# Kernel optimization log

Measured on AMD Instinct MI355X. Metric: run time of the kernel, lower is better.

## Reference

```python
import jax, jax.numpy as jnp
import numpy as np

N_TV_ITER = 20      # fixed Chambolle iteration count (skimage early-stops via eps; fixed for jit)
TV_WEIGHT = 0.1


def _div(p):
    # negative adjoint of forward-difference gradient (skimage convention)
    d = -(p[0] + p[1])
    d = d.at[1:, :].add(p[0, :-1, :])
    d = d.at[:, 1:].add(p[1, :, :-1])
    return d


def tv_chambolle_2d(image):
    """skimage.restoration.denoise_tv_chambolle on a single 2D image, weight=0.1."""
    tau = 0.25  # 1 / (2 * ndim)

    def step(p, _):
        out = image + _div(p)
        gy = jnp.zeros_like(out).at[:-1, :].set(out[1:, :] - out[:-1, :])
        gx = jnp.zeros_like(out).at[:, :-1].set(out[:, 1:] - out[:, :-1])
        norm = jnp.sqrt(gy * gy + gx * gx)
        g = jnp.stack([gy, gx])
        p = (p - tau * g) / (1.0 + (tau / TV_WEIGHT) * norm)
        return p, None

    p0 = jnp.zeros((2,) + image.shape, image.dtype)
    p, _ = jax.lax.scan(step, p0, None, length=N_TV_ITER)
    return image + _div(p)


def tv_denoise(img):  # [B,C,H,W], vmapped over B*C (replaces the CPU python loop)
    B, C, H, W = img.shape
    out = jax.vmap(tv_chambolle_2d)(img.reshape(B * C, H, W))
    return out.reshape(B, C, H, W)


def conv(x, w, stride=1, groups=1):
    pad = w.shape[2] // 2  # 'same'-style padding for odd kernels, 0 for 1x1
    return jax.lax.conv_general_dilated(
        x, w, (stride, stride), [(pad, pad), (pad, pad)],
        dimension_numbers=('NCHW', 'OIHW', 'NCHW'),
        feature_group_count=groups)


def haar_ll(x):
    # one level of pywt wavedec2('haar') LL band: 0.5 * sum over each 2x2 block
    return 0.5 * (x[..., ::2, ::2] + x[..., ::2, 1::2] + x[..., 1::2, ::2] + x[..., 1::2, 1::2])


def backbone(x, stem_w, dw_pw):
    # stride-32, 1280-channel EfficientNet-B0-style feature extractor
    x = jax.nn.silu(conv(x, stem_w, stride=2))
    for dw, pw in dw_pw:
        x = jax.nn.silu(conv(x, dw, stride=2, groups=dw.shape[0]))
        x = jax.nn.silu(conv(x, pw))
    return x


def setup_inputs() -> dict:
    key = jax.random.key(0)
    ks = jax.random.split(key, 16)
    B, H, W = 4, 512, 512

    def w(k, o, i, kh, kw):
        return jax.random.normal(k, (o, i, kh, kw), jnp.float32) * (1.0 / np.sqrt(i * kh * kw))

    return {
        "img": jax.random.normal(ks[0], (B, 1, H, W), jnp.float32),
        "stem_w": w(ks[1], 32, 1, 3, 3),
        "dw1_w": w(ks[2], 32, 1, 3, 3),  "pw1_w": w(ks[3], 64, 32, 1, 1),
        "dw2_w": w(ks[4], 64, 1, 3, 3),  "pw2_w": w(ks[5], 128, 64, 1, 1),
        "dw3_w": w(ks[6], 128, 1, 3, 3), "pw3_w": w(ks[7], 256, 128, 1, 1),
        "dw4_w": w(ks[8], 256, 1, 3, 3), "pw4_w": w(ks[9], 512, 256, 1, 1),
        "head_w": w(ks[10], 1280, 512, 1, 1),
        "proj_w": w(ks[11], 64, 1280, 1, 1),
        "proj_b": jnp.zeros((64,), jnp.float32),
        "final_w": w(ks[12], 1, 64, 1, 1),
        "final_b": jnp.zeros((1,), jnp.float32),
    }


def reference(img, stem_w, dw1_w, pw1_w, dw2_w, pw2_w, dw3_w, pw3_w, dw4_w, pw4_w,
              head_w, proj_w, proj_b, final_w, final_b):
    B, C, H, W = img.shape
    x = tv_denoise(img)                                     # fused TV Chambolle
    x = backbone(x, stem_w, [(dw1_w, pw1_w), (dw2_w, pw2_w), (dw3_w, pw3_w), (dw4_w, pw4_w)])
    x = jax.nn.silu(conv(x, head_w))                        # [B,1280,H/32,W/32]
    x = conv(x, proj_w) + proj_b[None, :, None, None]       # [B,64,H/32,W/32]
    x = jax.image.resize(x, (B, 64, H, W), method='bilinear')  # align_corners=False semantics
    ll = haar_ll(haar_ll(x))                                # 2-level Haar LL: [B,64,H/4,W/4]
    out = conv(ll, final_w) + final_b[None, :, None, None]  # [B,1,H/4,W/4]
    return out
```

## Files before the change

### kernel.cpp

```cpp
#include <hip/hip_runtime.h>
#include <math.h>

constexpr int BATCH = 4;
constexpr int IMG_H = 512, IMG_W = 512;
constexpr int IMG_HW = IMG_H * IMG_W;
constexpr int PSTR = BATCH * IMG_HW;

constexpr size_t O_PA   = 0;
constexpr size_t O_PB   = O_PA + 2 * (size_t)PSTR;
constexpr size_t O_DEN  = O_PB + 2 * (size_t)PSTR;
constexpr size_t O_A1   = O_DEN + (size_t)PSTR;
constexpr size_t O_A2   = O_A1 + 8388608;
constexpr size_t O_WT1  = O_A2 + 2097152;
constexpr size_t O_WT2  = O_WT1 + 32 * 64;
constexpr size_t O_WT3  = O_WT2 + 64 * 128;
constexpr size_t O_WT4  = O_WT3 + 128 * 256;
constexpr size_t O_WTH  = O_WT4 + 256 * 512;
constexpr size_t O_WCOMB= O_WTH + 512 * 1280;
constexpr size_t O_BCOMB= O_WCOMB + 1280;
constexpr size_t O_S    = O_BCOMB + 4;
constexpr size_t WS_FLOATS = O_S + 1024;

__device__ __forceinline__ float fast_rcp(float x) { return __builtin_amdgcn_rcpf(x); }
__device__ __forceinline__ float fast_sqrt(float x) { return __builtin_amdgcn_sqrtf(x); }
__device__ __forceinline__ float silu_f(float x) {
    float e = __builtin_amdgcn_exp2f(-1.44269504088896f * x);
    return x * fast_rcp(1.0f + e);
}
__device__ __forceinline__ int clampi(int v, int lo, int hi) {
    return v < lo ? lo : (v > hi ? hi : v);
}

template <int NST, bool FIRST, bool LAST>
__global__ __launch_bounds__(512) void tv_reg(const float* __restrict__ img,
                                              const float* __restrict__ pin,
                                              float* __restrict__ pout) {
    constexpr int ROWS = 7, NW = 8, HL = 10, TC = 44, TR = 32;
    __shared__ float bndP[512], bndO[512];
    const int tid = threadIdx.x;
    const int lane = tid & 63, w = tid >> 6;
    const int b = blockIdx.z;
    const int r0 = blockIdx.y * TR, c0 = blockIdx.x * TC;
    const int gj = c0 - HL + lane;
    const int gjc = clampi(gj, 0, 511);
    const int gib = r0 - HL + w * ROWS;
    const float* I = img + b * IMG_HW;
    const bool interior = (r0 - HL >= 1) && (r0 + NW * ROWS - HL <= 511) &&
                          (c0 - HL >= 1) && (c0 + 64 - HL <= 511);

    float rim[ROWS], rp0[ROWS], rp1[ROWS], ro[ROWS];
#pragma unroll
    for (int k = 0; k < ROWS; ++k) {
        int gi = clampi(gib + k, 0, 511);
        rim[k] = I[(gi << 9) + gjc];
    }
    if (!FIRST) {
        const float* P0 = pin + b * IMG_HW;
        const float* P1 = pin + PSTR + b * IMG_HW;
#pragma unroll
        for (int k = 0; k < ROWS; ++k) {
            int gi = clampi(gib + k, 0, 511);
            rp0[k] = P0[(gi << 9) + gjc];
            rp1[k] = P1[(gi << 9) + gjc];
        }
    }
    const bool gjpos = (gj > 0), gjlt = (gj < 511);

    int s0 = 0;
    if (FIRST) {
        bndO[tid] = rim[0];
        __syncthreads();
        float odn = (w < NW - 1) ? bndO[tid + 64] : 0.0f;
        if (interior) {
#pragma unroll
            for (int k = 0; k < ROWS; ++k) {
                float oR = __shfl_down(rim[k], 1);
                float od = (k < ROWS - 1) ? rim[k + 1] : odn;
                float gy = od - rim[k];
                float gx = oR - rim[k];
                float inv = fast_rcp(fmaf(2.5f, fast_sqrt(fmaf(gy, gy, gx * gx)), 1.0f));
                rp0[k] = -0.25f * gy * inv;
                rp1[k] = -0.25f * gx * inv;
            }
        } else {
#pragma unroll
            for (int k = 0; k < ROWS; ++k) {
                float oR = __shfl_down(rim[k], 1);
                float od = (k < ROWS - 1) ? rim[k + 1] : odn;
                int gi = gib + k;
                float gy = (gi < 511) ? od - rim[k] : 0.0f;
                float gx = gjlt ? oR - rim[k] : 0.0f;
                float inv = fast_rcp(fmaf(2.5f, fast_sqrt(fmaf(gy, gy, gx * gx)), 1.0f));
                rp0[k] = -0.25f * gy * inv;
                rp1[k] = -0.25f * gx * inv;
            }
        }
        s0 = 1;
    }

    for (int s = s0; s < NST; ++s) {
        bndP[tid] = rp0[ROWS - 1];
        __syncthreads();
        float pup0 = (w > 0) ? bndP[tid - 64] : 0.0f;
        if (interior) {
#pragma unroll
            for (int k = 0; k < ROWS; ++k) {
                float p1l = __shfl_up(rp1[k], 1);
                float pup = (k > 0) ? rp0[k - 1] : pup0;
                ro[k] = rim[k] - rp0[k] - rp1[k] + pup + p1l;
            }
            bndO[tid] = ro[0];
            __syncthreads();
            float odn = (w < NW - 1) ? bndO[tid + 64] : 0.0f;
#pragma unroll
            for (int k = 0; k < ROWS; ++k) {
                float oR = __shfl_down(ro[k], 1);
                float od = (k < ROWS - 1) ? ro[k + 1] : odn;
                float gy = od - ro[k];
                float gx = oR - ro[k];
                float inv = fast_rcp(fmaf(2.5f, fast_sqrt(fmaf(gy, gy, gx * gx)), 1.0f));
                rp0[k] = (rp0[k] - 0.25f * gy) * inv;
                rp1[k] = (rp1[k] - 0.25f * gx) * inv;
            }
        } else {
#pragma unroll
            for (int k = 0; k < ROWS; ++k) {
                float p1l = __shfl_up(rp1[k], 1);
                float o = rim[k] - rp0[k] - rp1[k];
                float pup = (k > 0) ? rp0[k - 1] : pup0;
                int gi = gib + k;
                if (gi > 0) o += pup;
                if (gjpos) o += p1l;
                ro[k] = o;
            }
            bndO[tid] = ro[0];
            __syncthreads();
            float odn = (w < NW - 1) ? bndO[tid + 64] : 0.0f;
#pragma unroll
            for (int k = 0; k < ROWS; ++k) {
                float oR = __shfl_down(ro[k], 1);
                float od = (k < ROWS - 1) ? ro[k + 1] : odn;
                int gi = gib + k;
                float gy = (gi < 511) ? od - ro[k] : 0.0f;
                float gx = gjlt ? oR - ro[k] : 0.0f;
                float inv = fast_rcp(fmaf(2.5f, fast_sqrt(fmaf(gy, gy, gx * gx)), 1.0f));
                rp0[k] = (rp0[k] - 0.25f * gy) * inv;
                rp1[k] = (rp1[k] - 0.25f * gx) * inv;
            }
        }
    }

    const bool cst = (lane >= HL && lane < HL + TC && gj < 512);
    if (LAST) {
        bndP[tid] = rp0[ROWS - 1];
        __syncthreads();
        float pup0 = (w > 0) ? bndP[tid - 64] : 0.0f;
        float* D = pout + b * IMG_HW;
#pragma unroll
        for (int k = 0; k < ROWS; ++k) {
            float p1l = __shfl_up(rp1[k], 1);
            int gi = gib + k;
            int rk = w * ROWS + k;
            float o = rim[k] - rp0[k] - rp1[k];
            float pup = (k > 0) ? rp0[k - 1] : pup0;
            if (gi > 0) o += pup;
            if (gjpos) o += p1l;
            if (rk >= HL && rk < HL + TR && cst) D[(gi << 9) + gj] = o;
        }
    } else {
        float* Q0 = pout + b * IMG_HW;
        float* Q1 = pout + PSTR + b * IMG_HW;
#pragma unroll
        for (int k = 0; k < ROWS; ++k) {
            int rk = w * ROWS + k;
            int gi = gib + k;
            if (rk >= HL && rk < HL + TR && cst) {
                Q0[(gi << 9) + gj] = rp0[k];
                Q1[(gi << 9) + gj] = rp1[k];
            }
        }
    }
}

__global__ __launch_bounds__(256) void stem_dw1_pw1(const float* __restrict__ den,
                                                    const float* __restrict__ stemw,
                                                    const float* __restrict__ dw1w,
                                                    const float* __restrict__ pw1T,
                                                    float* __restrict__ out) {
    __shared__ float sDen[35 * 36];
    __shared__ float sStem[8 * 323];
    __shared__ float sDw[32 * 64];
    __shared__ float sW[576];
    __shared__ __align__(16) float sWp[2048];
    const int tid = threadIdx.x;
    const int b = blockIdx.z;
    const int r0 = blockIdx.y * 32, c0 = blockIdx.x * 32;
    const float* D = den + b * IMG_HW;
    for (int e = tid; e < 576; e += 256) sW[e] = (e < 288) ? stemw[e] : dw1w[e - 288];
    for (int e = tid; e < 2048; e += 256) sWp[e] = pw1T[e];
    for (int e = tid; e < 35 * 35; e += 256) {
        int li = e / 35, lj = e % 35;
        int gi = r0 - 3 + li, gjj = c0 - 3 + lj;
        sDen[li * 36 + lj] = (gi >= 0 && gjj >= 0) ? D[(gi << 9) + gjj] : 0.0f;
    }
    __syncthreads();

    for (int g = 0; g < 4; ++g) {
        if (g) __syncthreads();
        for (int e = tid; e < 2312; e += 256) {
            int pos = e >> 3, cl = e & 7;
            int sy = pos / 17, sx = pos % 17;
            int c = 8 * g + cl;
            const float* wc = &sW[c * 9];
            const float* dbase = &sDen[(2 * sy) * 36 + 2 * sx];
            float a = 0.0f;
#pragma unroll
            for (int ky = 0; ky < 3; ++ky)
#pragma unroll
                for (int kx = 0; kx < 3; ++kx)
                    a = fmaf(wc[ky * 3 + kx], dbase[ky * 36 + kx], a);
            sStem[cl * 323 + sy * 19 + sx] = silu_f(a);
        }
        __syncthreads();
        for (int e = tid; e < 512; e += 256) {
            int cl = e >> 6, dy = (e >> 3) & 7, dx = e & 7;
            int c = 8 * g + cl;
            float acc = 0.0f;
#pragma unroll
            for (int ky = 0; ky < 3; ++ky)
#pragma unroll
                for (int kx = 0; kx < 3; ++kx) {
                    int sgy = (r0 >> 1) - 1 + 2 * dy + ky;
                    int sgx = (c0 >> 1) - 1 + 2 * dx + kx;
                    float v = (sgy >= 0 && sgx >= 0)
                        ? sStem[cl * 323 + (2 * dy + ky) * 19 + 2 * dx + kx] : 0.0f;
                    acc = fmaf(sW[288 + c * 9 + ky * 3 + kx], v, acc);
                }
            sDw[c * 64 + (dy << 3) + dx] = silu_f(acc);
        }
    }
    __syncthreads();

    const int px = tid & 63, oc0 = (tid >> 6) * 16;
    float acc[16];
#pragma unroll
    for (int j = 0; j < 16; ++j) acc[j] = 0.0f;
    for (int ic = 0; ic < 32; ++ic) {
        float v = sDw[ic * 64 + px];
        const float* wr = &sWp[ic * 64 + oc0];
#pragma unroll
        for (int q = 0; q < 4; ++q) {
            float4 w4 = *(const float4*)(wr + q * 4);
            acc[q * 4 + 0] = fmaf(v, w4.x, acc[q * 4 + 0]);
            acc[q * 4 + 1] = fmaf(v, w4.y, acc[q * 4 + 1]);
            acc[q * 4 + 2] = fmaf(v, w4.z, acc[q * 4 + 2]);
            acc[q * 4 + 3] = fmaf(v, w4.w, acc[q * 4 + 3]);
        }
    }
    const int gpos = ((r0 >> 2) + (px >> 3)) * 128 + (c0 >> 2) + (px & 7);
    float* ob = out + (size_t)b * 64 * 16384 + (size_t)oc0 * 16384 + gpos;
#pragma unroll
    for (int j = 0; j < 16; ++j) ob[(size_t)j * 16384] = silu_f(acc[j]);
}

template <int C, int HIN>
__global__ __launch_bounds__(256) void dw_kernel(const float* __restrict__ in,
                                                 const float* __restrict__ w,
                                                 float* __restrict__ out) {
    constexpr int HO = HIN / 2;
    int t = blockIdx.x * 256 + threadIdx.x;
    int x = t % HO;
    int y = (t / HO) % HO;
    int c = (t / (HO * HO)) % C;
    int b = t / (HO * HO * C);
    const float* I = in + ((size_t)(b * C + c)) * (HIN * HIN);
    const float* wc = w + c * 9;
    int iy = 2 * y - 1, ix = 2 * x - 1;
    float acc = 0.0f;
#pragma unroll
    for (int ky = 0; ky < 3; ++ky)
#pragma unroll
        for (int kx = 0; kx < 3; ++kx) {
            int yy = iy + ky, xx = ix + kx;
            float vv = (yy >= 0 && xx >= 0) ? I[yy * HIN + xx] : 0.0f;
            acc = fmaf(wc[ky * 3 + kx], vv, acc);
        }
    out[t] = silu_f(acc);
}

template <int C, int HIN>
__global__ __launch_bounds__(256) void dw_reduce2_kernel(const float* __restrict__ part,
                                                         const float* __restrict__ w,
                                                         float* __restrict__ out) {
    constexpr int HO = HIN / 2;
    int t = blockIdx.x * 256 + threadIdx.x;
    int x = t % HO;
    int y = (t / HO) % HO;
    int c = (t / (HO * HO)) % C;
    int b = t / (HO * HO * C);
    const float* Ia = part + ((size_t)(b * C + c)) * (HIN * HIN);
    const float* Ib = Ia + (size_t)BATCH * C * HIN * HIN;
    const float* wc = w + c * 9;
    int iy = 2 * y - 1, ix = 2 * x - 1;
    float acc = 0.0f;
#pragma unroll
    for (int ky = 0; ky < 3; ++ky)
#pragma unroll
        for (int kx = 0; kx < 3; ++kx) {
            int yy = iy + ky, xx = ix + kx;
            float vv = 0.0f;
            if (yy >= 0 && xx >= 0) {
                int o = yy * HIN + xx;
                vv = silu_f(Ia[o] + Ib[o]);
            }
            acc = fmaf(wc[ky * 3 + kx], vv, acc);
        }
    out[t] = silu_f(acc);
}

template <int ICT, int NSIN, int NSPLIT, int OC, bool SILU>
__global__ __launch_bounds__(256) void pw_gemm(const float* __restrict__ in,
                                               const float* __restrict__ wT,
                                               float* __restrict__ out,
                                               int HW) {
    constexpr int KC = 32, TP = 64, TOC = 64, OPT = 4, PPT = 4;
    constexpr int KS = ICT / NSPLIT;
    constexpr int NC = KS / KC;
    constexpr int NOG = TOC / OPT;
    constexpr int PV4 = KC * TP / 4 / 256;
    constexpr int WV4 = KC * TOC / 4 / 256;
    static_assert(KS % KC == 0, "split");
    __shared__ __align__(16) float sPx[2][KC * TP];
    __shared__ __align__(16) float sW[2][KC * TOC];
    const int tid = threadIdx.x;
    const int zb = blockIdx.z;
    const int b = zb / NSPLIT, ks = zb % NSPLIT;
    const int p0 = blockIdx.x * TP;
    const int oc0 = blockIdx.y * TOC;
    const int ocg = tid % NOG, pxg = tid / NOG;
    const size_t instride = (size_t)BATCH * ICT * HW;
    const float* gin0 = in + ((size_t)b * ICT + ks * KS) * HW + p0;
    const float* gw0  = wT + ((size_t)(ks * KS)) * OC + oc0;

    float4 rp[PV4], rw[WV4];
    auto load_chunk = [&](int cc) {
        const float* gin = gin0 + (size_t)cc * KC * HW;
#pragma unroll
        for (int i = 0; i < PV4; ++i) {
            int e = tid + i * 256;
            int row = e / (TP / 4), col = e % (TP / 4);
            const float* base = gin + (size_t)row * HW + col * 4;
            float4 a = *(const float4*)base;
#pragma unroll
            for (int s = 1; s < NSIN; ++s) {
                float4 t4 = *(const float4*)(base + (size_t)s * instride);
                a.x += t4.x; a.y += t4.y; a.z += t4.z; a.w += t4.w;
            }
            if (NSIN > 1) {
                a.x = silu_f(a.x); a.y = silu_f(a.y);
                a.z = silu_f(a.z); a.w = silu_f(a.w);
            }
            rp[i] = a;
        }
        const float* gw = gw0 + (size_t)cc * KC * OC;
#pragma unroll
        for (int i = 0; i < WV4; ++i) {
            int e = tid + i * 256;
            int row = e / (TOC / 4), col = e % (TOC / 4);
            rw[i] = *(const float4*)(gw + (size_t)row * OC + col * 4);
        }
    };
    auto store_chunk = [&](int buf) {
#pragma unroll
        for (int i = 0; i < PV4; ++i) ((float4*)sPx[buf])[tid + i * 256] = rp[i];
#pragma unroll
        for (int i = 0; i < WV4; ++i) ((float4*)sW[buf])[tid + i * 256] = rw[i];
    };

    float acc[OPT][PPT];
#pragma unroll
    for (int o = 0; o < OPT; ++o)
#pragma unroll
        for (int p = 0; p < PPT; ++p) acc[o][p] = 0.0f;

    load_chunk(0);
    store_chunk(0);
    __syncthreads();
    for (int cc = 0; cc < NC; ++cc) {
        if (cc + 1 < NC) load_chunk(cc + 1);
        const int buf = cc & 1;
#pragma unroll 4
        for (int k = 0; k < KC; ++k) {
            float4 pv = *(const float4*)&sPx[buf][k * TP + pxg * PPT];
            float4 wv = *(const float4*)&sW[buf][k * TOC + ocg * OPT];
            float w0 = wv.x, w1 = wv.y, w2 = wv.z, w3 = wv.w;
            acc[0][0] = fmaf(pv.x, w0, acc[0][0]);
            acc[0][1] = fmaf(pv.y, w0, acc[0][1]);
            acc[0][2] = fmaf(pv.z, w0, acc[0][2]);
            acc[0][3] = fmaf(pv.w, w0, acc[0][3]);
            acc[1][0] = fmaf(pv.x, w1, acc[1][0]);
            acc[1][1] = fmaf(pv.y, w1, acc[1][1]);
            acc[1][2] = fmaf(pv.z, w1, acc[1][2]);
            acc[1][3] = fmaf(pv.w, w1, acc[1][3]);
            acc[2][0] = fmaf(pv.x, w2, acc[2][0]);
            acc[2][1] = fmaf(pv.y, w2, acc[2][1]);
            acc[2][2] = fmaf(pv.z, w2, acc[2][2]);
            acc[2][3] = fmaf(pv.w, w2, acc[2][3]);
            acc[3][0] = fmaf(pv.x, w3, acc[3][0]);
            acc[3][1] = fmaf(pv.y, w3, acc[3][1]);
            acc[3][2] = fmaf(pv.z, w3, acc[3][2]);
            acc[3][3] = fmaf(pv.w, w3, acc[3][3]);
        }
        if (cc + 1 < NC) {
            store_chunk((cc + 1) & 1);
            __syncthreads();
        }
    }

    float* ob;
    if (NSPLIT == 1)
        ob = out + ((size_t)(b * OC + oc0 + ocg * OPT)) * HW + p0 + pxg * PPT;
    else
        ob = out + (((size_t)(ks * BATCH + b)) * OC + oc0 + ocg * OPT) * HW + p0 + pxg * PPT;
#pragma unroll
    for (int o = 0; o < OPT; ++o) {
        float4 r;
        r.x = SILU ? silu_f(acc[o][0]) : acc[o][0];
        r.y = SILU ? silu_f(acc[o][1]) : acc[o][1];
        r.z = SILU ? silu_f(acc[o][2]) : acc[o][2];
        r.w = SILU ? silu_f(acc[o][3]) : acc[o][3];
        *(float4*)(ob + (size_t)o * HW) = r;
    }
}

__global__ __launch_bounds__(256) void prep_kernel(const float* __restrict__ pw1,
                                                   const float* __restrict__ pw2,
                                                   const float* __restrict__ pw3,
                                                   const float* __restrict__ pw4,
                                                   const float* __restrict__ headw,
                                                   const float* __restrict__ projw,
                                                   const float* __restrict__ projb,
                                                   const float* __restrict__ finalw,
                                                   const float* __restrict__ finalb,
                                                   float* __restrict__ ws) {
    __shared__ float t[32][33];
    const int bx = blockIdx.x;
    const float* src;
    float* dst;
    int R, C, tr, tc;
    if (bx < 640) {
        src = headw; dst = ws + O_WTH; R = 1280; C = 512;
        tr = bx >> 4; tc = bx & 15;
    } else if (bx < 768) {
        int e = bx - 640;
        src = pw4; dst = ws + O_WT4; R = 512; C = 256;
        tr = e >> 3; tc = e & 7;
    } else if (bx < 800) {
        int e = bx - 768;
        src = pw3; dst = ws + O_WT3; R = 256; C = 128;
        tr = e >> 2; tc = e & 3;
    } else if (bx < 808) {
        int e = bx - 800;
        src = pw2; dst = ws + O_WT2; R = 128; C = 64;
        tr = e >> 1; tc = e & 1;
    } else if (bx < 810) {
        int e = bx - 808;
        src = pw1; dst = ws + O_WT1; R = 64; C = 32;
        tr = e; tc = 0;
    } else if (bx < 815) {
        int k = (bx - 810) * 256 + threadIdx.x;
        if (k < 1280) {
            float a = 0.0f;
            for (int ch = 0; ch < 64; ++ch) a = fmaf(finalw[ch], projw[ch * 1280 + k], a);
            ws[O_WCOMB + k] = a;
        }
        return;
    } else {
        if (threadIdx.x == 0) {
            float a = 0.0f;
            for (int ch = 0; ch < 64; ++ch) a = fmaf(finalw[ch], projb[ch], a);
            ws[O_BCOMB] = a;
        }
        return;
    }
    const int tx = threadIdx.x & 31, ty = threadIdx.x >> 5;
#pragma unroll
    for (int j = 0; j < 4; ++j)
        t[ty + j * 8][tx] = src[(size_t)(tr * 32 + ty + j * 8) * C + tc * 32 + tx];
    __syncthreads();
#pragma unroll
    for (int j = 0; j < 4; ++j)
        dst[(size_t)(tc * 32 + ty + j * 8) * R + tr * 32 + tx] = t[tx][ty + j * 8];
}

__global__ __launch_bounds__(256) void tail_head(const float* __restrict__ part,
                                                 const float* __restrict__ wcomb,
                                                 const float* __restrict__ bcomb,
                                                 float* __restrict__ s) {
    __shared__ float red[256];
    constexpr size_t PS = (size_t)4 * 1280 * 256;
    int b = blockIdx.x >> 4;
    int px0 = (blockIdx.x & 15) << 4;
    int px = threadIdx.x & 15, kg = threadIdx.x >> 4;
    const float* h0 = part + (size_t)b * 1280 * 256 + px0 + px;
    float acc = 0.0f;
    int k0 = kg * 80;
    for (int k = k0; k < k0 + 80; ++k) {
        size_t off = (size_t)k * 256;
        float v = silu_f(h0[off] + h0[off + PS] + h0[off + 2 * PS] + h0[off + 3 * PS]);
        acc = fmaf(wcomb[k], v, acc);
    }
    red[threadIdx.x] = acc;
    __syncthreads();
    if (threadIdx.x < 16) {
        float a = bcomb[0];
#pragma unroll
        for (int g = 0; g < 16; ++g) a += red[g * 16 + threadIdx.x];
        s[b * 256 + px0 + threadIdx.x] = a;
    }
}

__global__ __launch_bounds__(256) void resize_haar(const float* __restrict__ s,
                                                   const float* __restrict__ finalb,
                                                   float* __restrict__ out) {
    int t = blockIdx.x * 256 + threadIdx.x;
    int c = t & 127, r = (t >> 7) & 127, b = t >> 14;
    const float* S = s + b * 256;
    float acc = 0.0f;
#pragma unroll
    for (int j = 0; j < 4; ++j) {
        float sy = ((4 * r + j) + 0.5f) * (1.0f / 32.0f) - 0.5f;
        int y0 = (int)floorf(sy);
        float fy = sy - (float)y0;
        int ya = y0 < 0 ? 0 : y0;
        int yb = (y0 + 1) > 15 ? 15 : (y0 + 1);
#pragma unroll
        for (int i = 0; i < 4; ++i) {
            float sx = ((4 * c + i) + 0.5f) * (1.0f / 32.0f) - 0.5f;
            int x0 = (int)floorf(sx);
            float fx = sx - (float)x0;
            int xa = x0 < 0 ? 0 : x0;
            int xb = (x0 + 1) > 15 ? 15 : (x0 + 1);
            float v0 = S[ya * 16 + xa] * (1.0f - fx) + S[ya * 16 + xb] * fx;
            float v1 = S[yb * 16 + xa] * (1.0f - fx) + S[yb * 16 + xb] * fx;
            acc += v0 * (1.0f - fy) + v1 * fy;
        }
    }
    out[t] = 0.25f * acc + finalb[0];
}

extern "C" void kernel_launch(void* const* d_in, const int* in_sizes, int n_in,
                              void* d_out, int out_size, void* d_ws, size_t ws_size,
                              hipStream_t stream) {
    if (ws_size < WS_FLOATS * sizeof(float)) return;

    const float* img    = (const float*)d_in[0];
    const float* stem_w = (const float*)d_in[1];
    const float* dw1_w  = (const float*)d_in[2];
    const float* pw1_w  = (const float*)d_in[3];
    const float* dw2_w  = (const float*)d_in[4];
    const float* pw2_w  = (const float*)d_in[5];
    const float* dw3_w  = (const float*)d_in[6];
    const float* pw3_w  = (const float*)d_in[7];
    const float* dw4_w  = (const float*)d_in[8];
    const float* pw4_w  = (const float*)d_in[9];
    const float* head_w = (const float*)d_in[10];
    const float* proj_w = (const float*)d_in[11];
    const float* proj_b = (const float*)d_in[12];
    const float* final_w= (const float*)d_in[13];
    const float* final_b= (const float*)d_in[14];
    float* ws  = (float*)d_ws;
    float* out = (float*)d_out;

    prep_kernel<<<816, 256, 0, stream>>>(pw1_w, pw2_w, pw3_w, pw4_w, head_w,
                                         proj_w, proj_b, final_w, final_b, ws);

    dim3 tvg(12, 16, 4);
    tv_reg<10, true,  false><<<tvg, 512, 0, stream>>>(img, img,       ws + O_PA);
    tv_reg<10, false, true ><<<tvg, 512, 0, stream>>>(img, ws + O_PA, ws + O_DEN);

    stem_dw1_pw1<<<dim3(16, 16, 4), 256, 0, stream>>>(ws + O_DEN, stem_w, dw1_w,
                                                      ws + O_WT1, ws + O_A1);

    dw_kernel<64, 128><<<4096, 256, 0, stream>>>(ws + O_A1, dw2_w, ws + O_A2);
    pw_gemm<64, 1, 2, 128, false><<<dim3(64, 2, 8), 256, 0, stream>>>(ws + O_A2, ws + O_WT2, ws + O_PA, 4096);

    dw_reduce2_kernel<128, 64><<<2048, 256, 0, stream>>>(ws + O_PA, dw3_w, ws + O_A1);
    pw_gemm<128, 1, 2, 256, false><<<dim3(16, 4, 8), 256, 0, stream>>>(ws + O_A1, ws + O_WT3, ws + O_PA, 1024);

    dw_reduce2_kernel<256, 32><<<1024, 256, 0, stream>>>(ws + O_PA, dw4_w, ws + O_A2);
    pw_gemm<256, 1, 4, 512, false><<<dim3(4, 8, 16), 256, 0, stream>>>(ws + O_A2, ws + O_WT4, ws + O_PA, 256);

    pw_gemm<512, 4, 4, 1280, false><<<dim3(4, 20, 16), 256, 0, stream>>>(ws + O_PA, ws + O_WTH, ws + O_A1, 256);
    tail_head<<<64, 256, 0, stream>>>(ws + O_A1, ws + O_WCOMB, ws + O_BCOMB, ws + O_S);

    resize_haar<<<256, 256, 0, stream>>>(ws + O_S, final_b, out);
}
```

Measured before the change: 252.3 us.

## Shrink TV tiles to fill more CUs and fold weight prep into first TV launch

The TV tile shrinks from 32 to 28 output rows (6 rows per wave), which raises the grid from 16 to 19 row-blocks so more blocks spread across the CUs. The separate weight-transpose and combine prep kernel is removed. Its work now runs in 2 extra row-blocks of the first TV launch, overlapping with TV compute and saving one launch. The cost is more halo recomputation per output and extra bounds checks on rows past the image edge.

```diff
diff --git a/kernel.cpp b/kernel.cpp
--- a/kernel.cpp
+++ b/kernel.cpp
@@ -34,9 +34,73 @@
 template <int NST, bool FIRST, bool LAST>
 __global__ __launch_bounds__(512) void tv_reg(const float* __restrict__ img,
                                               const float* __restrict__ pin,
-                                              float* __restrict__ pout) {
-    constexpr int ROWS = 7, NW = 8, HL = 10, TC = 44, TR = 32;
+                                              float* __restrict__ pout,
+                                              const float* __restrict__ pw1,
+                                              const float* __restrict__ pw2,
+                                              const float* __restrict__ pw3,
+                                              const float* __restrict__ pw4,
+                                              const float* __restrict__ headw,
+                                              const float* __restrict__ projw,
+                                              const float* __restrict__ projb,
+                                              const float* __restrict__ finalw,
+                                              float* __restrict__ ws) {
+    constexpr int ROWS = 6, NW = 8, HL = 10, TC = 44, TR = 28;
+    constexpr int TVY = 19;
     __shared__ float bndP[512], bndO[512];
+
+    if constexpr (FIRST) {
+        if (blockIdx.y >= TVY) {
+            __shared__ float tt[32][33];
+            const int tid = threadIdx.x;
+            const int pid = ((blockIdx.y - TVY) * 4 + blockIdx.z) * 12 + blockIdx.x;
+            for (int t = pid; t < 814; t += 96) {
+                const float* src = nullptr; float* dst = nullptr;
+                int C = 0, R = 0, tr = 0, tc = 0;
+                if (t < 640) {
+                    src = headw; dst = ws + O_WTH; R = 1280; C = 512; tr = t >> 4; tc = t & 15;
+                } else if (t < 768) {
+                    int e = t - 640; src = pw4; dst = ws + O_WT4; R = 512; C = 256; tr = e >> 3; tc = e & 7;
+                } else if (t < 800) {
+                    int e = t - 768; src = pw3; dst = ws + O_WT3; R = 256; C = 128; tr = e >> 2; tc = e & 3;
+                } else if (t < 808) {
+                    int e = t - 800; src = pw2; dst = ws + O_WT2; R = 128; C = 64; tr = e >> 1; tc = e & 1;
+                } else if (t < 810) {
+                    int e = t - 808; src = pw1; dst = ws + O_WT1; R = 64; C = 32; tr = e; tc = 0;
+                }
+                const int tx = tid & 31, ty = tid >> 5;
+                __syncthreads();
+                if (src) {
+#pragma unroll
+                    for (int j = 0; j < 2; ++j)
+                        tt[ty + j * 16][tx] =
+                            src[(size_t)(tr * 32 + ty + j * 16) * C + tc * 32 + tx];
+                }
+                __syncthreads();
+                if (src) {
+#pragma unroll
+                    for (int j = 0; j < 2; ++j)
+                        dst[(size_t)(tc * 32 + ty + j * 16) * R + tr * 32 + tx] =
+                            tt[tx][ty + j * 16];
+                } else if (t < 813) {
+                    int k = (t - 810) * 512 + tid;
+                    if (k < 1280) {
+                        float a = 0.0f;
+                        for (int ch = 0; ch < 64; ++ch)
+                            a = fmaf(finalw[ch], projw[ch * 1280 + k], a);
+                        ws[O_WCOMB + k] = a;
+                    }
+                } else {
+                    if (tid == 0) {
+                        float a = 0.0f;
+                        for (int ch = 0; ch < 64; ++ch) a = fmaf(finalw[ch], projb[ch], a);
+                        ws[O_BCOMB] = a;
+                    }
+                }
+            }
+            return;
+        }
+    }
+
     const int tid = threadIdx.x;
     const int lane = tid & 63, w = tid >> 6;
     const int b = blockIdx.z;
@@ -165,7 +229,7 @@
             float pup = (k > 0) ? rp0[k - 1] : pup0;
             if (gi > 0) o += pup;
             if (gjpos) o += p1l;
-            if (rk >= HL && rk < HL + TR && cst) D[(gi << 9) + gj] = o;
+            if (rk >= HL && rk < HL + TR && cst && gi < 512) D[(gi << 9) + gj] = o;
         }
     } else {
         float* Q0 = pout + b * IMG_HW;
@@ -174,7 +238,7 @@
         for (int k = 0; k < ROWS; ++k) {
             int rk = w * ROWS + k;
             int gi = gib + k;
-            if (rk >= HL && rk < HL + TR && cst) {
+            if (rk >= HL && rk < HL + TR && cst && gi < 512) {
                 Q0[(gi << 9) + gj] = rp0[k];
                 Q1[(gi << 9) + gj] = rp1[k];
             }
@@ -433,66 +497,6 @@
     }
 }
 
-__global__ __launch_bounds__(256) void prep_kernel(const float* __restrict__ pw1,
-                                                   const float* __restrict__ pw2,
-                                                   const float* __restrict__ pw3,
-                                                   const float* __restrict__ pw4,
-                                                   const float* __restrict__ headw,
-                                                   const float* __restrict__ projw,
-                                                   const float* __restrict__ projb,
-                                                   const float* __restrict__ finalw,
-                                                   const float* __restrict__ finalb,
-                                                   float* __restrict__ ws) {
-    __shared__ float t[32][33];
-    const int bx = blockIdx.x;
-    const float* src;
-    float* dst;
-    int R, C, tr, tc;
-    if (bx < 640) {
-        src = headw; dst = ws + O_WTH; R = 1280; C = 512;
-        tr = bx >> 4; tc = bx & 15;
-    } else if (bx < 768) {
-        int e = bx - 640;
-        src = pw4; dst = ws + O_WT4; R = 512; C = 256;
-        tr = e >> 3; tc = e & 7;
-    } else if (bx < 800) {
-        int e = bx - 768;
-        src = pw3; dst = ws + O_WT3; R = 256; C = 128;
-        tr = e >> 2; tc = e & 3;
-    } else if (bx < 808) {
-        int e = bx - 800;
-        src = pw2; dst = ws + O_WT2; R = 128; C = 64;
-        tr = e >> 1; tc = e & 1;
-    } else if (bx < 810) {
-        int e = bx - 808;
-        src = pw1; dst = ws + O_WT1; R = 64; C = 32;
-        tr = e; tc = 0;
-    } else if (bx < 815) {
-        int k = (bx - 810) * 256 + threadIdx.x;
-        if (k < 1280) {
-            float a = 0.0f;
-            for (int ch = 0; ch < 64; ++ch) a = fmaf(finalw[ch], projw[ch * 1280 + k], a);
-            ws[O_WCOMB + k] = a;
-        }
-        return;
-    } else {
-        if (threadIdx.x == 0) {
-            float a = 0.0f;
-            for (int ch = 0; ch < 64; ++ch) a = fmaf(finalw[ch], projb[ch], a);
-            ws[O_BCOMB] = a;
-        }
-        return;
-    }
-    const int tx = threadIdx.x & 31, ty = threadIdx.x >> 5;
-#pragma unroll
-    for (int j = 0; j < 4; ++j)
-        t[ty + j * 8][tx] = src[(size_t)(tr * 32 + ty + j * 8) * C + tc * 32 + tx];
-    __syncthreads();
-#pragma unroll
-    for (int j = 0; j < 4; ++j)
-        dst[(size_t)(tc * 32 + ty + j * 8) * R + tr * 32 + tx] = t[tx][ty + j * 8];
-}
-
 __global__ __launch_bounds__(256) void tail_head(const float* __restrict__ part,
                                                  const float* __restrict__ wcomb,
                                                  const float* __restrict__ bcomb,
@@ -572,12 +576,13 @@
     float* ws  = (float*)d_ws;
     float* out = (float*)d_out;
 
-    prep_kernel<<<816, 256, 0, stream>>>(pw1_w, pw2_w, pw3_w, pw4_w, head_w,
-                                         proj_w, proj_b, final_w, final_b, ws);
-
-    dim3 tvg(12, 16, 4);
-    tv_reg<10, true,  false><<<tvg, 512, 0, stream>>>(img, img,       ws + O_PA);
-    tv_reg<10, false, true ><<<tvg, 512, 0, stream>>>(img, ws + O_PA, ws + O_DEN);
+    dim3 tvg1(12, 21, 4), tvg2(12, 19, 4);
+    tv_reg<10, true,  false><<<tvg1, 512, 0, stream>>>(
+        img, img, ws + O_PA,
+        pw1_w, pw2_w, pw3_w, pw4_w, head_w, proj_w, proj_b, final_w, ws);
+    tv_reg<10, false, true ><<<tvg2, 512, 0, stream>>>(
+        img, ws + O_PA, ws + O_DEN,
+        nullptr, nullptr, nullptr, nullptr, nullptr, nullptr, nullptr, nullptr, ws);
 
     stem_dw1_pw1<<<dim3(16, 16, 4), 256, 0, stream>>>(ws + O_DEN, stem_w, dw1_w,
                                                       ws + O_WT1, ws + O_A1);
```

Result: no change. 253.3 us (+0.4%).
